# Kernel tuning notes

Measured on AMD Instinct MI355X. Metric: run time of the kernel, lower is better.

The kernel has to match this reference:

```python
import jax, jax.numpy as jnp
import numpy as np

N, D, E, OUT = 100000, 128, 600000, 128


def setup_inputs() -> dict:
    key = jax.random.key(0)
    k1, k2, k3, k4, k5 = jax.random.split(key, 5)
    x = jax.random.normal(k1, (N, D), dtype=jnp.float32)
    # Linear params (stored as [in, out]; y = h @ W + b, same math as nn.Linear)
    W = jax.random.normal(k2, (D, OUT), dtype=jnp.float32) * (1.0 / np.sqrt(D))
    b = jax.random.normal(k3, (OUT,), dtype=jnp.float32) * 0.01
    # Flattened ragged neighbor lists as COO edges: node edge_dst[e] aggregates x[edge_src[e]]
    edge_src = jax.random.randint(k4, (E,), 0, N, dtype=jnp.int32)
    edge_dst = jnp.sort(jax.random.randint(k5, (E,), 0, N, dtype=jnp.int32))
    return {"x": x, "W": W, "b": b, "edge_src": edge_src, "edge_dst": edge_dst}


def reference(x, W, b, edge_src, edge_dst):
    n = x.shape[0]
    # segment-mean of neighbor features per destination node
    neigh_sum = jax.ops.segment_sum(x[edge_src], edge_dst, num_segments=n)  # [N, D]
    deg = jax.ops.segment_sum(jnp.ones((edge_dst.shape[0],), x.dtype), edge_dst, num_segments=n)  # [N]
    # nodes with no neighbors keep zero mean (matches `if neigh:` branch)
    neigh_mean = neigh_sum / jnp.maximum(deg, 1.0)[:, None]
    h = x + neigh_mean
    return jax.nn.relu(h @ W + b)
```

## Files before the change

### kernel.cpp

```cpp
#include <hip/hip_runtime.h>
#include <hip/hip_bf16.h>


#define FD  128
#define BR  64
#define HSB 136

typedef __attribute__((ext_vector_type(8))) short bf16x8;
typedef __attribute__((ext_vector_type(4))) float f32x4;

__device__ __forceinline__ short f2bf(float f) {
    unsigned u = __float_as_uint(f);
    return (short)((u + 0x7FFFu + ((u >> 16) & 1u)) >> 16);
}
__device__ __forceinline__ float bf2f(short s) {
    return __uint_as_float(((unsigned)(unsigned short)s) << 16);
}

__global__ __launch_bounds__(256) void prep_full_kernel(
    const float* __restrict__ x, const float* __restrict__ W,
    const int* __restrict__ edst, int* __restrict__ rp,
    short* __restrict__ pkW, short* __restrict__ xb, int N, int E)
{
    const int gid = blockIdx.x * 256 + threadIdx.x;
    const int nth = gridDim.x * 256;

    const int nv = N * FD / 8;
    for (int i = gid; i < nv; i += nth) {
        float4 f0 = *(const float4*)(x + (size_t)i * 8);
        float4 f1 = *(const float4*)(x + (size_t)i * 8 + 4);
        short tmp[8] = {f2bf(f0.x), f2bf(f0.y), f2bf(f0.z), f2bf(f0.w),
                        f2bf(f1.x), f2bf(f1.y), f2bf(f1.z), f2bf(f1.w)};
        *(bf16x8*)(xb + (size_t)i * 8) = *(bf16x8*)tmp;
    }
    for (int e = gid; e < E; e += nth) {
        int cur = edst[e];
        int prev = e ? edst[e - 1] : -1;
        for (int v = prev + 1; v <= cur; ++v) rp[v] = e;
        if (e == E - 1)
            for (int v = cur + 1; v <= N; ++v) rp[v] = E;
    }
    if (gid < 2048) {
        int wave = gid >> 9, rem = gid & 511;
        int ct = rem >> 8, rem2 = rem & 255;
        int kt = rem2 >> 6, lane = rem2 & 63;
        int q = lane >> 4, lr = lane & 15;
        int col = wave * 32 + ct * 16 + lr;
        int k0 = kt * 32 + q * 8;
        short tmp[8];
#pragma unroll
        for (int e2 = 0; e2 < 8; ++e2)
            tmp[e2] = f2bf(W[(size_t)(k0 + e2) * FD + col]);
        *(bf16x8*)(pkW + (size_t)gid * 8) = *(bf16x8*)tmp;
    }
}

__global__ __launch_bounds__(256) void meanagg_main2_kernel(
    const short* __restrict__ xb, const short* __restrict__ pkW,
    const float* __restrict__ bias, const int* __restrict__ esrc,
    const int* __restrict__ rp, float* __restrict__ out, int N, int E)
{
    __shared__ short shb[BR * HSB];
    __shared__ int seg[BR + 1];

    const int t = threadIdx.x;
    const int base = blockIdx.x * BR;

    if (t < BR + 1) {
        int idx = base + t;
        seg[t] = rp[idx > N ? N : idx];
    }
    __syncthreads();

    const int wave = t >> 6;
    const int lane = t & 63;
    const int qw = lane >> 4;
    const int ql = lane & 15;
    const int qb = qw << 4;
    const int rowbase = wave * 16;

    {
        int rb0 = rowbase + qw;
        int r0  = base + rb0;
        int s = (r0 < N) ? seg[rb0] : 0;
        int e = (r0 < N) ? seg[rb0 + 1] : 0;
        int srcv_n = (s + ql < e) ? esrc[s + ql] : 0;
        bf16x8 xv_n = {0, 0, 0, 0, 0, 0, 0, 0};
        if (r0 < N) xv_n = *(const bf16x8*)(xb + (size_t)r0 * FD + 8 * ql);

        for (int it = 0; it < 4; ++it) {
            const int cur_rb = rowbase + it * 4 + qw;
            const int cur_r  = base + cur_rb;
            const int cs0 = s, ce = e;
            int srcv = srcv_n;
            const bf16x8 xv = xv_n;

            if (it < 3) {
                int nrb = rowbase + (it + 1) * 4 + qw;
                int nr  = base + nrb;
                s = (nr < N) ? seg[nrb] : 0;
                e = (nr < N) ? seg[nrb + 1] : 0;
                srcv_n = (s + ql < e) ? esrc[s + ql] : 0;
                bf16x8 z = {0, 0, 0, 0, 0, 0, 0, 0};
                xv_n = z;
                if (nr < N) xv_n = *(const bf16x8*)(xb + (size_t)nr * FD + 8 * ql);
            }

            if (cur_r < N) {
                float a[8];
#pragma unroll
                for (int p = 0; p < 8; ++p) a[p] = 0.f;

                for (int cs = cs0; cs < ce; cs += 16) {
                    int m = ce - cs; if (m > 16) m = 16;
                    if (cs != cs0)
                        srcv = (cs + ql < ce) ? esrc[cs + ql] : 0;
                    for (int j0 = 0; j0 < m; j0 += 6) {
                        uint4 v[6];
#pragma unroll
                        for (int u = 0; u < 6; ++u) {
                            int jj = j0 + u;
                            int idx = __shfl(srcv, qb + (jj & 15));
                            if (jj >= m) idx = 0;
                            v[u] = *(const uint4*)(xb + (size_t)idx * FD + 8 * ql);
                        }
#pragma unroll
                        for (int u = 0; u < 6; ++u) {
                            float f = (j0 + u < m) ? 1.f : 0.f;
                            unsigned w;
                            w = v[u].x;
                            a[0] = fmaf(__uint_as_float(w << 16), f, a[0]);
                            a[1] = fmaf(__uint_as_float(w & 0xFFFF0000u), f, a[1]);
                            w = v[u].y;
                            a[2] = fmaf(__uint_as_float(w << 16), f, a[2]);
                            a[3] = fmaf(__uint_as_float(w & 0xFFFF0000u), f, a[3]);
                            w = v[u].z;
                            a[4] = fmaf(__uint_as_float(w << 16), f, a[4]);
                            a[5] = fmaf(__uint_as_float(w & 0xFFFF0000u), f, a[5]);
                            w = v[u].w;
                            a[6] = fmaf(__uint_as_float(w << 16), f, a[6]);
                            a[7] = fmaf(__uint_as_float(w & 0xFFFF0000u), f, a[7]);
                        }
                    }
                }
                int deg = ce - cs0;
                float inv = 1.0f / (float)(deg > 0 ? deg : 1);
                short hb[8];
#pragma unroll
                for (int p = 0; p < 8; ++p)
                    hb[p] = f2bf(bf2f(xv[p]) + a[p] * inv);
                *(bf16x8*)(shb + cur_rb * HSB + 8 * ql) = *(bf16x8*)hb;
            }
        }
    }
    __syncthreads();

    const int lr = lane & 15;
    const int q  = lane >> 4;
    const int colb = wave * 32;

    bf16x8 bfr[2][4];
#pragma unroll
    for (int ct = 0; ct < 2; ++ct)
#pragma unroll
        for (int kt = 0; kt < 4; ++kt) {
            int f = ((wave * 2 + ct) * 4 + kt) * 64 + lane;
            bfr[ct][kt] = *(const bf16x8*)(pkW + (size_t)f * 8);
        }

    f32x4 acc[4][2];
#pragma unroll
    for (int rt = 0; rt < 4; ++rt) {
        acc[rt][0] = (f32x4){0.f, 0.f, 0.f, 0.f};
        acc[rt][1] = (f32x4){0.f, 0.f, 0.f, 0.f};
    }

#pragma unroll
    for (int rt = 0; rt < 4; ++rt)
#pragma unroll
        for (int kt = 0; kt < 4; ++kt) {
            bf16x8 av = *(const bf16x8*)(shb + (rt * 16 + lr) * HSB + kt * 32 + q * 8);
            acc[rt][0] = __builtin_amdgcn_mfma_f32_16x16x32_bf16(av, bfr[0][kt], acc[rt][0], 0, 0, 0);
            acc[rt][1] = __builtin_amdgcn_mfma_f32_16x16x32_bf16(av, bfr[1][kt], acc[rt][1], 0, 0, 0);
        }

    const float b0 = bias[colb + lr];
    const float b1 = bias[colb + 16 + lr];

#pragma unroll
    for (int rt = 0; rt < 4; ++rt)
#pragma unroll
        for (int j = 0; j < 4; ++j) {
            int row = base + rt * 16 + q * 4 + j;
            if (row < N) {
                float v0 = acc[rt][0][j] + b0; v0 = v0 > 0.f ? v0 : 0.f;
                float v1 = acc[rt][1][j] + b1; v1 = v1 > 0.f ? v1 : 0.f;
                out[(size_t)row * FD + colb + lr]      = v0;
                out[(size_t)row * FD + colb + 16 + lr] = v1;
            }
        }
}

__global__ __launch_bounds__(256) void prep_kernel(
    const float* __restrict__ W, const int* __restrict__ edst,
    int* __restrict__ rp, short* __restrict__ pkW, int N, int E)
{
    int gid = blockIdx.x * 256 + threadIdx.x;
    if (gid < E) {
        int cur = edst[gid];
        int prev = gid ? edst[gid - 1] : -1;
        for (int v = prev + 1; v <= cur; ++v) rp[v] = gid;
        if (gid == E - 1)
            for (int v = cur + 1; v <= N; ++v) rp[v] = E;
    }
    if (gid < 2048) {
        int wave = gid >> 9, rem = gid & 511;
        int ct = rem >> 8, rem2 = rem & 255;
        int kt = rem2 >> 6, lane = rem2 & 63;
        int q = lane >> 4, lr = lane & 15;
        int col = wave * 32 + ct * 16 + lr;
        int k0 = kt * 32 + q * 8;
        short tmp[8];
#pragma unroll
        for (int e = 0; e < 8; ++e)
            tmp[e] = f2bf(W[(size_t)(k0 + e) * FD + col]);
        *(bf16x8*)(pkW + (size_t)gid * 8) = *(bf16x8*)tmp;
    }
}

__global__ __launch_bounds__(256) void meanagg_main_kernel(
    const float* __restrict__ x, const short* __restrict__ pkW,
    const float* __restrict__ bias, const int* __restrict__ esrc,
    const int* __restrict__ rp, float* __restrict__ out, int N, int E)
{
    __shared__ short shb[BR * HSB];
    __shared__ int seg[BR + 1];

    const int t = threadIdx.x;
    const int base = blockIdx.x * BR;

    if (t < BR + 1) {
        int idx = base + t;
        seg[t] = rp[idx > N ? N : idx];
    }
    __syncthreads();

    const int wave = t >> 6;
    const int lane = t & 63;
    const int sw = lane >> 5;
    const int sl = lane & 31;
    const int lb = sw << 5;
    const int rowbase = wave * 16;

    {
        int rb0 = rowbase + sw;
        int r0  = base + rb0;
        int s0  = (r0 < N) ? seg[rb0] : 0;
        int e0  = (r0 < N) ? seg[rb0 + 1] : 0;
        int src_next = (s0 + sl < e0) ? esrc[s0 + sl] : 0;
        float4 xv_next = make_float4(0.f, 0.f, 0.f, 0.f);
        if (r0 < N) xv_next = *(const float4*)(x + (size_t)r0 * FD + 4 * sl);

        int s = s0, e = e0;
        for (int it = 0; it < 8; ++it) {
            const int cur_rb = rowbase + it * 2 + sw;
            const int cur_r  = base + cur_rb;
            const int cur_s  = s, cur_e = e;
            const int src_l  = src_next;
            const float4 xv  = xv_next;

            if (it < 7) {
                int nrb = rowbase + (it + 1) * 2 + sw;
                int nr  = base + nrb;
                s = (nr < N) ? seg[nrb] : 0;
                e = (nr < N) ? seg[nrb + 1] : 0;
                src_next = (s + sl < e) ? esrc[s + sl] : 0;
                xv_next = make_float4(0.f, 0.f, 0.f, 0.f);
                if (nr < N) xv_next = *(const float4*)(x + (size_t)nr * FD + 4 * sl);
            }

            if (cur_r < N) {
                float4 a0 = make_float4(0.f, 0.f, 0.f, 0.f), a1 = a0;
                int srcv = src_l;
                for (int cs = cur_s; cs < cur_e; cs += 32) {
                    int m = cur_e - cs; if (m > 32) m = 32;
                    if (cs != cur_s)
                        srcv = (cs + sl < cur_e) ? esrc[cs + sl] : 0;
                    for (int j0 = 0; j0 < m; j0 += 8) {
                        const int rem = m - j0;
                        float4 v[8];
#pragma unroll
                        for (int u = 0; u < 8; ++u) {
                            int idx = __shfl(srcv, lb + ((j0 + u) & 31));
                            v[u] = *(const float4*)(x + (size_t)idx * FD + 4 * sl);
                        }
#pragma unroll
                        for (int u = 0; u < 8; ++u) {
                            float f = (u < rem) ? 1.f : 0.f;
                            float4* A = (u & 1) ? &a1 : &a0;
                            A->x = fmaf(v[u].x, f, A->x);
                            A->y = fmaf(v[u].y, f, A->y);
                            A->z = fmaf(v[u].z, f, A->z);
                            A->w = fmaf(v[u].w, f, A->w);
                        }
                    }
                }
                int deg = cur_e - cur_s;
                float inv = 1.0f / (float)(deg > 0 ? deg : 1);
                short4 hb;
                hb.x = f2bf(xv.x + (a0.x + a1.x) * inv);
                hb.y = f2bf(xv.y + (a0.y + a1.y) * inv);
                hb.z = f2bf(xv.z + (a0.z + a1.z) * inv);
                hb.w = f2bf(xv.w + (a0.w + a1.w) * inv);
                *(short4*)(shb + cur_rb * HSB + 4 * sl) = hb;
            }
        }
    }
    __syncthreads();

    const int lr = lane & 15;
    const int q  = lane >> 4;
    const int colb = wave * 32;

    bf16x8 bfr[2][4];
#pragma unroll
    for (int ct = 0; ct < 2; ++ct)
#pragma unroll
        for (int kt = 0; kt < 4; ++kt) {
            int f = ((wave * 2 + ct) * 4 + kt) * 64 + lane;
            bfr[ct][kt] = *(const bf16x8*)(pkW + (size_t)f * 8);
        }

    f32x4 acc[4][2];
#pragma unroll
    for (int rt = 0; rt < 4; ++rt) {
        acc[rt][0] = (f32x4){0.f, 0.f, 0.f, 0.f};
        acc[rt][1] = (f32x4){0.f, 0.f, 0.f, 0.f};
    }

#pragma unroll
    for (int rt = 0; rt < 4; ++rt)
#pragma unroll
        for (int kt = 0; kt < 4; ++kt) {
            bf16x8 av = *(const bf16x8*)(shb + (rt * 16 + lr) * HSB + kt * 32 + q * 8);
            acc[rt][0] = __builtin_amdgcn_mfma_f32_16x16x32_bf16(av, bfr[0][kt], acc[rt][0], 0, 0, 0);
            acc[rt][1] = __builtin_amdgcn_mfma_f32_16x16x32_bf16(av, bfr[1][kt], acc[rt][1], 0, 0, 0);
        }

    const float b0 = bias[colb + lr];
    const float b1 = bias[colb + 16 + lr];

#pragma unroll
    for (int rt = 0; rt < 4; ++rt)
#pragma unroll
        for (int j = 0; j < 4; ++j) {
            int row = base + rt * 16 + q * 4 + j;
            if (row < N) {
                float v0 = acc[rt][0][j] + b0; v0 = v0 > 0.f ? v0 : 0.f;
                float v1 = acc[rt][1][j] + b1; v1 = v1 > 0.f ? v1 : 0.f;
                out[(size_t)row * FD + colb + lr]      = v0;
                out[(size_t)row * FD + colb + 16 + lr] = v1;
            }
        }
}

__global__ __launch_bounds__(256) void meanagg_fused_kernel(
    const float* __restrict__ x, const float* __restrict__ W,
    const float* __restrict__ bias, const int* __restrict__ esrc,
    const int* __restrict__ edst, float* __restrict__ out, int N, int E)
{
    __shared__ short shb[BR * HSB];
    __shared__ int seg[BR + 1];

    const int t = threadIdx.x;
    const int base = blockIdx.x * BR;

    if (t < BR + 1) {
        int v = base + t;
        int lo = 0, hi = E;
        while (lo < hi) {
            int mid = (lo + hi) >> 1;
            if (edst[mid] < v) lo = mid + 1; else hi = mid;
        }
        seg[t] = lo;
    }
    __syncthreads();

    const int wave = t >> 6;
    const int lane = t & 63;
    const int sw = lane >> 5;
    const int sl = lane & 31;
    const int lb = sw << 5;
    const int rowbase = wave * 16;

    for (int it = 0; it < 8; ++it) {
        int cur_rb = rowbase + it * 2 + sw;
        int cur_r  = base + cur_rb;
        if (cur_r >= N) break;
        int cur_s = seg[cur_rb], cur_e = seg[cur_rb + 1];
        float4 a0 = make_float4(0.f, 0.f, 0.f, 0.f), a1 = a0;
        for (int cs = cur_s; cs < cur_e; cs += 32) {
            int m = cur_e - cs; if (m > 32) m = 32;
            int srcv = (cs + sl < cur_e) ? esrc[cs + sl] : 0;
            for (int j0 = 0; j0 < m; j0 += 8) {
                const int rem = m - j0;
#pragma unroll
                for (int u = 0; u < 8; ++u) {
                    int idx = __shfl(srcv, lb + ((j0 + u) & 31));
                    float4 v = *(const float4*)(x + (size_t)idx * FD + 4 * sl);
                    float f = (u < rem) ? 1.f : 0.f;
                    float4* A = (u & 1) ? &a1 : &a0;
                    A->x = fmaf(v.x, f, A->x);
                    A->y = fmaf(v.y, f, A->y);
                    A->z = fmaf(v.z, f, A->z);
                    A->w = fmaf(v.w, f, A->w);
                }
            }
        }
        float4 xv = *(const float4*)(x + (size_t)cur_r * FD + 4 * sl);
        int deg = cur_e - cur_s;
        float inv = 1.0f / (float)(deg > 0 ? deg : 1);
        short4 hb;
        hb.x = f2bf(xv.x + (a0.x + a1.x) * inv);
        hb.y = f2bf(xv.y + (a0.y + a1.y) * inv);
        hb.z = f2bf(xv.z + (a0.z + a1.z) * inv);
        hb.w = f2bf(xv.w + (a0.w + a1.w) * inv);
        *(short4*)(shb + cur_rb * HSB + 4 * sl) = hb;
    }
    __syncthreads();

    const int lr = lane & 15;
    const int q  = lane >> 4;
    const int colb = wave * 32;

    bf16x8 bfr[2][4];
#pragma unroll
    for (int ct = 0; ct < 2; ++ct) {
        int col = colb + ct * 16 + lr;
#pragma unroll
        for (int kt = 0; kt < 4; ++kt) {
            bf16x8 f;
#pragma unroll
            for (int e = 0; e < 8; ++e)
                f[e] = f2bf(W[(size_t)(kt * 32 + q * 8 + e) * FD + col]);
            bfr[ct][kt] = f;
        }
    }

    f32x4 acc[4][2];
#pragma unroll
    for (int rt = 0; rt < 4; ++rt) {
        acc[rt][0] = (f32x4){0.f, 0.f, 0.f, 0.f};
        acc[rt][1] = (f32x4){0.f, 0.f, 0.f, 0.f};
    }

#pragma unroll
    for (int rt = 0; rt < 4; ++rt)
#pragma unroll
        for (int kt = 0; kt < 4; ++kt) {
            bf16x8 av = *(const bf16x8*)(shb + (rt * 16 + lr) * HSB + kt * 32 + q * 8);
            acc[rt][0] = __builtin_amdgcn_mfma_f32_16x16x32_bf16(av, bfr[0][kt], acc[rt][0], 0, 0, 0);
            acc[rt][1] = __builtin_amdgcn_mfma_f32_16x16x32_bf16(av, bfr[1][kt], acc[rt][1], 0, 0, 0);
        }

    const float b0 = bias[colb + lr];
    const float b1 = bias[colb + 16 + lr];

#pragma unroll
    for (int rt = 0; rt < 4; ++rt)
#pragma unroll
        for (int j = 0; j < 4; ++j) {
            int row = base + rt * 16 + q * 4 + j;
            if (row < N) {
                float v0 = acc[rt][0][j] + b0; v0 = v0 > 0.f ? v0 : 0.f;
                float v1 = acc[rt][1][j] + b1; v1 = v1 > 0.f ? v1 : 0.f;
                out[(size_t)row * FD + colb + lr]      = v0;
                out[(size_t)row * FD + colb + 16 + lr] = v1;
            }
        }
}

extern "C" void kernel_launch(void* const* d_in, const int* in_sizes, int n_in,
                              void* d_out, int out_size, void* d_ws, size_t ws_size,
                              hipStream_t stream) {
    const float* x    = (const float*)d_in[0];
    const float* W    = (const float*)d_in[1];
    const float* bias = (const float*)d_in[2];
    const int* esrc   = (const int*)d_in[3];
    const int* edst   = (const int*)d_in[4];
    float* out        = (float*)d_out;

    int N = in_sizes[0] / FD;
    int E = in_sizes[3];
    int blocks = (N + BR - 1) / BR;

    size_t rp_bytes = (size_t)(N + 1) * 4;
    size_t pk_off   = (rp_bytes + 511) & ~(size_t)511;
    size_t xb_off   = (pk_off + 2048 * 8 * 2 + 511) & ~(size_t)511;
    size_t need_med = pk_off + 2048 * 8 * 2;
    size_t need_big = xb_off + (size_t)N * FD * 2;

    if (ws_size >= need_big) {
        int* rp    = (int*)d_ws;
        short* pkW = (short*)((char*)d_ws + pk_off);
        short* xb  = (short*)((char*)d_ws + xb_off);
        prep_full_kernel<<<2048, 256, 0, stream>>>(x, W, edst, rp, pkW, xb, N, E);
        meanagg_main2_kernel<<<blocks, 256, 0, stream>>>(xb, pkW, bias, esrc, rp, out, N, E);
    } else if (ws_size >= need_med) {
        int* rp    = (int*)d_ws;
        short* pkW = (short*)((char*)d_ws + pk_off);
        int pblocks = (E + 255) / 256;
        prep_kernel<<<pblocks, 256, 0, stream>>>(W, edst, rp, pkW, N, E);
        meanagg_main_kernel<<<blocks, 256, 0, stream>>>(x, pkW, bias, esrc, rp, out, N, E);
    } else {
        meanagg_fused_kernel<<<blocks, 256, 0, stream>>>(x, W, bias, esrc, edst, out, N, E);
    }
}
```

Before: 57.65 us.

## Halve rows per block and issue both rows' neighbor gathers upfront

The main aggregation kernel now handles 32 rows per block instead of 64, which doubles the grid. Each 16-lane group processes two rows and issues the first 8 neighbor gathers for both rows before accumulating either, replacing the old sequential 4-iteration prefetch loop. Higher-degree rows fall back to a tail loop that gathers 8 at a time. The aim is more memory-level parallelism and more blocks in flight to hide gather latency. The cost is more register pressure from 16 outstanding uint4 loads, and each block loads W fragments for half as many rows.

```diff
diff --git a/kernel.cpp b/kernel.cpp
--- a/kernel.cpp
+++ b/kernel.cpp
@@ -3,7 +3,8 @@
 
 
 #define FD  128
-#define BR  64
+#define BR  32
+#define BRF 64
 #define HSB 136
 
 typedef __attribute__((ext_vector_type(8))) short bf16x8;
@@ -39,6 +40,9 @@
         for (int v = prev + 1; v <= cur; ++v) rp[v] = e;
         if (e == E - 1)
             for (int v = cur + 1; v <= N; ++v) rp[v] = E;
+    }
+    if (E == 0) {
+        for (int v = gid; v <= N; v += nth) rp[v] = 0;
     }
     if (gid < 2048) {
         int wave = gid >> 9, rem = gid & 511;
@@ -55,7 +59,76 @@
     }
 }
 
-__global__ __launch_bounds__(256) void meanagg_main2_kernel(
+__device__ __forceinline__ void issue8(const short* __restrict__ xb, int srcv,
+                                       int qb, int ql, int j0, int m, uint4 v[8])
+{
+#pragma unroll
+    for (int u = 0; u < 8; ++u) {
+        int jj = j0 + u;
+        int idx = __shfl(srcv, qb + (jj & 15));
+        if (jj >= m) idx = 0;
+        v[u] = *(const uint4*)(xb + (size_t)idx * FD + 8 * ql);
+    }
+}
+
+__device__ __forceinline__ void acc8(const uint4 v[8], int c, float2 a[4])
+{
+#pragma unroll
+    for (int u = 0; u < 8; ++u) {
+        float f = (u < c) ? 1.f : 0.f;
+        unsigned w;
+        w = v[u].x;
+        a[0].x = fmaf(__uint_as_float(w << 16), f, a[0].x);
+        a[0].y = fmaf(__uint_as_float(w & 0xFFFF0000u), f, a[0].y);
+        w = v[u].y;
+        a[1].x = fmaf(__uint_as_float(w << 16), f, a[1].x);
+        a[1].y = fmaf(__uint_as_float(w & 0xFFFF0000u), f, a[1].y);
+        w = v[u].z;
+        a[2].x = fmaf(__uint_as_float(w << 16), f, a[2].x);
+        a[2].y = fmaf(__uint_as_float(w & 0xFFFF0000u), f, a[2].y);
+        w = v[u].w;
+        a[3].x = fmaf(__uint_as_float(w << 16), f, a[3].x);
+        a[3].y = fmaf(__uint_as_float(w & 0xFFFF0000u), f, a[3].y);
+    }
+}
+
+__device__ __forceinline__ void row_tail(const short* __restrict__ xb,
+                                         const int* __restrict__ esrc,
+                                         int s, int e, int srcv,
+                                         int qb, int ql, float2 a[4])
+{
+    int deg = e - s;
+    if (deg > 8) {
+        uint4 v2[8];
+        int m16 = deg < 16 ? deg : 16;
+        issue8(xb, srcv, qb, ql, 8, m16, v2);
+        acc8(v2, m16 - 8, a);
+        for (int cs = s + 16; cs < e; cs += 16) {
+            int m = e - cs; if (m > 16) m = 16;
+            int sv = (cs + ql < e) ? esrc[cs + ql] : 0;
+            for (int j0 = 0; j0 < m; j0 += 8) {
+                issue8(xb, sv, qb, ql, j0, m, v2);
+                int c = m - j0; if (c > 8) c = 8;
+                acc8(v2, c, a);
+            }
+        }
+    }
+}
+
+__device__ __forceinline__ void finalize_row(short* shb, int rb, int ql,
+                                             const bf16x8 xv, const float2 a[4], int deg)
+{
+    float inv = 1.0f / (float)(deg > 0 ? deg : 1);
+    short hb[8];
+#pragma unroll
+    for (int k = 0; k < 4; ++k) {
+        hb[2 * k]     = f2bf(bf2f(xv[2 * k])     + a[k].x * inv);
+        hb[2 * k + 1] = f2bf(bf2f(xv[2 * k + 1]) + a[k].y * inv);
+    }
+    *(bf16x8*)(shb + rb * HSB + 8 * ql) = *(bf16x8*)hb;
+}
+
+__global__ __launch_bounds__(256) void meanagg_main3_kernel(
     const short* __restrict__ xb, const short* __restrict__ pkW,
     const float* __restrict__ bias, const int* __restrict__ esrc,
     const int* __restrict__ rp, float* __restrict__ out, int N, int E)
@@ -77,82 +150,38 @@
     const int qw = lane >> 4;
     const int ql = lane & 15;
     const int qb = qw << 4;
-    const int rowbase = wave * 16;
-
-    {
-        int rb0 = rowbase + qw;
-        int r0  = base + rb0;
-        int s = (r0 < N) ? seg[rb0] : 0;
-        int e = (r0 < N) ? seg[rb0 + 1] : 0;
-        int srcv_n = (s + ql < e) ? esrc[s + ql] : 0;
-        bf16x8 xv_n = {0, 0, 0, 0, 0, 0, 0, 0};
-        if (r0 < N) xv_n = *(const bf16x8*)(xb + (size_t)r0 * FD + 8 * ql);
-
-        for (int it = 0; it < 4; ++it) {
-            const int cur_rb = rowbase + it * 4 + qw;
-            const int cur_r  = base + cur_rb;
-            const int cs0 = s, ce = e;
-            int srcv = srcv_n;
-            const bf16x8 xv = xv_n;
-
-            if (it < 3) {
-                int nrb = rowbase + (it + 1) * 4 + qw;
-                int nr  = base + nrb;
-                s = (nr < N) ? seg[nrb] : 0;
-                e = (nr < N) ? seg[nrb + 1] : 0;
-                srcv_n = (s + ql < e) ? esrc[s + ql] : 0;
-                bf16x8 z = {0, 0, 0, 0, 0, 0, 0, 0};
-                xv_n = z;
-                if (nr < N) xv_n = *(const bf16x8*)(xb + (size_t)nr * FD + 8 * ql);
-            }
-
-            if (cur_r < N) {
-                float a[8];
-#pragma unroll
-                for (int p = 0; p < 8; ++p) a[p] = 0.f;
-
-                for (int cs = cs0; cs < ce; cs += 16) {
-                    int m = ce - cs; if (m > 16) m = 16;
-                    if (cs != cs0)
-                        srcv = (cs + ql < ce) ? esrc[cs + ql] : 0;
-                    for (int j0 = 0; j0 < m; j0 += 6) {
-                        uint4 v[6];
-#pragma unroll
-                        for (int u = 0; u < 6; ++u) {
-                            int jj = j0 + u;
-                            int idx = __shfl(srcv, qb + (jj & 15));
-                            if (jj >= m) idx = 0;
-                            v[u] = *(const uint4*)(xb + (size_t)idx * FD + 8 * ql);
-                        }
-#pragma unroll
-                        for (int u = 0; u < 6; ++u) {
-                            float f = (j0 + u < m) ? 1.f : 0.f;
-                            unsigned w;
-                            w = v[u].x;
-                            a[0] = fmaf(__uint_as_float(w << 16), f, a[0]);
-                            a[1] = fmaf(__uint_as_float(w & 0xFFFF0000u), f, a[1]);
-                            w = v[u].y;
-                            a[2] = fmaf(__uint_as_float(w << 16), f, a[2]);
-                            a[3] = fmaf(__uint_as_float(w & 0xFFFF0000u), f, a[3]);
-                            w = v[u].z;
-                            a[4] = fmaf(__uint_as_float(w << 16), f, a[4]);
-                            a[5] = fmaf(__uint_as_float(w & 0xFFFF0000u), f, a[5]);
-                            w = v[u].w;
-                            a[6] = fmaf(__uint_as_float(w << 16), f, a[6]);
-                            a[7] = fmaf(__uint_as_float(w & 0xFFFF0000u), f, a[7]);
-                        }
-                    }
-                }
-                int deg = ce - cs0;
-                float inv = 1.0f / (float)(deg > 0 ? deg : 1);
-                short hb[8];
-#pragma unroll
-                for (int p = 0; p < 8; ++p)
-                    hb[p] = f2bf(bf2f(xv[p]) + a[p] * inv);
-                *(bf16x8*)(shb + cur_rb * HSB + 8 * ql) = *(bf16x8*)hb;
-            }
-        }
-    }
+
+    const int rb0 = wave * 8 + qw;
+    const int rb1 = rb0 + 4;
+    const int r0 = base + rb0, r1 = base + rb1;
+
+    const int s0 = seg[rb0], e0 = seg[rb0 + 1];
+    const int s1 = seg[rb1], e1 = seg[rb1 + 1];
+
+    int srcv0 = (s0 + ql < e0) ? esrc[s0 + ql] : 0;
+    int srcv1 = (s1 + ql < e1) ? esrc[s1 + ql] : 0;
+    bf16x8 xv0 = {0, 0, 0, 0, 0, 0, 0, 0}, xv1 = xv0;
+    if (r0 < N) xv0 = *(const bf16x8*)(xb + (size_t)r0 * FD + 8 * ql);
+    if (r1 < N) xv1 = *(const bf16x8*)(xb + (size_t)r1 * FD + 8 * ql);
+
+    const int deg0 = e0 - s0, deg1 = e1 - s1;
+    const int m0 = deg0 < 16 ? deg0 : 16;
+    const int m1 = deg1 < 16 ? deg1 : 16;
+
+    uint4 v0[8], v1[8];
+    issue8(xb, srcv0, qb, ql, 0, m0, v0);
+    issue8(xb, srcv1, qb, ql, 0, m1, v1);
+
+    float2 a[4] = {{0.f, 0.f}, {0.f, 0.f}, {0.f, 0.f}, {0.f, 0.f}};
+    acc8(v0, m0 < 8 ? m0 : 8, a);
+    row_tail(xb, esrc, s0, e0, srcv0, qb, ql, a);
+    finalize_row(shb, rb0, ql, xv0, a, deg0);
+
+    a[0] = a[1] = a[2] = a[3] = make_float2(0.f, 0.f);
+    acc8(v1, m1 < 8 ? m1 : 8, a);
+    row_tail(xb, esrc, s1, e1, srcv1, qb, ql, a);
+    finalize_row(shb, rb1, ql, xv1, a, deg1);
+
     __syncthreads();
 
     const int lr = lane & 15;
@@ -168,15 +197,15 @@
             bfr[ct][kt] = *(const bf16x8*)(pkW + (size_t)f * 8);
         }
 
-    f32x4 acc[4][2];
-#pragma unroll
-    for (int rt = 0; rt < 4; ++rt) {
+    f32x4 acc[2][2];
+#pragma unroll
+    for (int rt = 0; rt < 2; ++rt) {
         acc[rt][0] = (f32x4){0.f, 0.f, 0.f, 0.f};
         acc[rt][1] = (f32x4){0.f, 0.f, 0.f, 0.f};
     }
 
 #pragma unroll
-    for (int rt = 0; rt < 4; ++rt)
+    for (int rt = 0; rt < 2; ++rt)
 #pragma unroll
         for (int kt = 0; kt < 4; ++kt) {
             bf16x8 av = *(const bf16x8*)(shb + (rt * 16 + lr) * HSB + kt * 32 + q * 8);
@@ -188,15 +217,15 @@
     const float b1 = bias[colb + 16 + lr];
 
 #pragma unroll
-    for (int rt = 0; rt < 4; ++rt)
+    for (int rt = 0; rt < 2; ++rt)
 #pragma unroll
         for (int j = 0; j < 4; ++j) {
             int row = base + rt * 16 + q * 4 + j;
             if (row < N) {
-                float v0 = acc[rt][0][j] + b0; v0 = v0 > 0.f ? v0 : 0.f;
-                float v1 = acc[rt][1][j] + b1; v1 = v1 > 0.f ? v1 : 0.f;
-                out[(size_t)row * FD + colb + lr]      = v0;
-                out[(size_t)row * FD + colb + 16 + lr] = v1;
+                float o0 = acc[rt][0][j] + b0; o0 = o0 > 0.f ? o0 : 0.f;
+                float o1 = acc[rt][1][j] + b1; o1 = o1 > 0.f ? o1 : 0.f;
+                out[(size_t)row * FD + colb + lr]      = o0;
+                out[(size_t)row * FD + colb + 16 + lr] = o1;
             }
         }
 }
@@ -233,156 +262,15 @@
     const float* __restrict__ bias, const int* __restrict__ esrc,
     const int* __restrict__ rp, float* __restrict__ out, int N, int E)
 {
-    __shared__ short shb[BR * HSB];
-    __shared__ int seg[BR + 1];
+    __shared__ short shb[BRF * HSB];
+    __shared__ int seg[BRF + 1];
 
     const int t = threadIdx.x;
-    const int base = blockIdx.x * BR;
-
-    if (t < BR + 1) {
+    const int base = blockIdx.x * BRF;
+
+    if (t < BRF + 1) {
         int idx = base + t;
         seg[t] = rp[idx > N ? N : idx];
-    }
-    __syncthreads();
-
-    const int wave = t >> 6;
-    const int lane = t & 63;
-    const int sw = lane >> 5;
-    const int sl = lane & 31;
-    const int lb = sw << 5;
-    const int rowbase = wave * 16;
-
-    {
-        int rb0 = rowbase + sw;
-        int r0  = base + rb0;
-        int s0  = (r0 < N) ? seg[rb0] : 0;
-        int e0  = (r0 < N) ? seg[rb0 + 1] : 0;
-        int src_next = (s0 + sl < e0) ? esrc[s0 + sl] : 0;
-        float4 xv_next = make_float4(0.f, 0.f, 0.f, 0.f);
-        if (r0 < N) xv_next = *(const float4*)(x + (size_t)r0 * FD + 4 * sl);
-
-        int s = s0, e = e0;
-        for (int it = 0; it < 8; ++it) {
-            const int cur_rb = rowbase + it * 2 + sw;
-            const int cur_r  = base + cur_rb;
-            const int cur_s  = s, cur_e = e;
-            const int src_l  = src_next;
-            const float4 xv  = xv_next;
-
-            if (it < 7) {
-                int nrb = rowbase + (it + 1) * 2 + sw;
-                int nr  = base + nrb;
-                s = (nr < N) ? seg[nrb] : 0;
-                e = (nr < N) ? seg[nrb + 1] : 0;
-                src_next = (s + sl < e) ? esrc[s + sl] : 0;
-                xv_next = make_float4(0.f, 0.f, 0.f, 0.f);
-                if (nr < N) xv_next = *(const float4*)(x + (size_t)nr * FD + 4 * sl);
-            }
-
-            if (cur_r < N) {
-                float4 a0 = make_float4(0.f, 0.f, 0.f, 0.f), a1 = a0;
-                int srcv = src_l;
-                for (int cs = cur_s; cs < cur_e; cs += 32) {
-                    int m = cur_e - cs; if (m > 32) m = 32;
-                    if (cs != cur_s)
-                        srcv = (cs + sl < cur_e) ? esrc[cs + sl] : 0;
-                    for (int j0 = 0; j0 < m; j0 += 8) {
-                        const int rem = m - j0;
-                        float4 v[8];
-#pragma unroll
-                        for (int u = 0; u < 8; ++u) {
-                            int idx = __shfl(srcv, lb + ((j0 + u) & 31));
-                            v[u] = *(const float4*)(x + (size_t)idx * FD + 4 * sl);
-                        }
-#pragma unroll
-                        for (int u = 0; u < 8; ++u) {
-                            float f = (u < rem) ? 1.f : 0.f;
-                            float4* A = (u & 1) ? &a1 : &a0;
-                            A->x = fmaf(v[u].x, f, A->x);
-                            A->y = fmaf(v[u].y, f, A->y);
-                            A->z = fmaf(v[u].z, f, A->z);
-                            A->w = fmaf(v[u].w, f, A->w);
-                        }
-                    }
-                }
-                int deg = cur_e - cur_s;
-                float inv = 1.0f / (float)(deg > 0 ? deg : 1);
-                short4 hb;
-                hb.x = f2bf(xv.x + (a0.x + a1.x) * inv);
-                hb.y = f2bf(xv.y + (a0.y + a1.y) * inv);
-                hb.z = f2bf(xv.z + (a0.z + a1.z) * inv);
-                hb.w = f2bf(xv.w + (a0.w + a1.w) * inv);
-                *(short4*)(shb + cur_rb * HSB + 4 * sl) = hb;
-            }
-        }
-    }
-    __syncthreads();
-
-    const int lr = lane & 15;
-    const int q  = lane >> 4;
-    const int colb = wave * 32;
-
-    bf16x8 bfr[2][4];
-#pragma unroll
-    for (int ct = 0; ct < 2; ++ct)
-#pragma unroll
-        for (int kt = 0; kt < 4; ++kt) {
-            int f = ((wave * 2 + ct) * 4 + kt) * 64 + lane;
-            bfr[ct][kt] = *(const bf16x8*)(pkW + (size_t)f * 8);
-        }
-
-    f32x4 acc[4][2];
-#pragma unroll
-    for (int rt = 0; rt < 4; ++rt) {
-        acc[rt][0] = (f32x4){0.f, 0.f, 0.f, 0.f};
-        acc[rt][1] = (f32x4){0.f, 0.f, 0.f, 0.f};
-    }
-
-#pragma unroll
-    for (int rt = 0; rt < 4; ++rt)
-#pragma unroll
-        for (int kt = 0; kt < 4; ++kt) {
-            bf16x8 av = *(const bf16x8*)(shb + (rt * 16 + lr) * HSB + kt * 32 + q * 8);
-            acc[rt][0] = __builtin_amdgcn_mfma_f32_16x16x32_bf16(av, bfr[0][kt], acc[rt][0], 0, 0, 0);
-            acc[rt][1] = __builtin_amdgcn_mfma_f32_16x16x32_bf16(av, bfr[1][kt], acc[rt][1], 0, 0, 0);
-        }
-
-    const float b0 = bias[colb + lr];
-    const float b1 = bias[colb + 16 + lr];
-
-#pragma unroll
-    for (int rt = 0; rt < 4; ++rt)
-#pragma unroll
-        for (int j = 0; j < 4; ++j) {
-            int row = base + rt * 16 + q * 4 + j;
-            if (row < N) {
-                float v0 = acc[rt][0][j] + b0; v0 = v0 > 0.f ? v0 : 0.f;
-                float v1 = acc[rt][1][j] + b1; v1 = v1 > 0.f ? v1 : 0.f;
-                out[(size_t)row * FD + colb + lr]      = v0;
-                out[(size_t)row * FD + colb + 16 + lr] = v1;
-            }
-        }
-}
-
-__global__ __launch_bounds__(256) void meanagg_fused_kernel(
-    const float* __restrict__ x, const float* __restrict__ W,
-    const float* __restrict__ bias, const int* __restrict__ esrc,
-    const int* __restrict__ edst, float* __restrict__ out, int N, int E)
-{
-    __shared__ short shb[BR * HSB];
-    __shared__ int seg[BR + 1];
-
-    const int t = threadIdx.x;
-    const int base = blockIdx.x * BR;
-
-    if (t < BR + 1) {
-        int v = base + t;
-        int lo = 0, hi = E;
-        while (lo < hi) {
-            int mid = (lo + hi) >> 1;
-            if (edst[mid] < v) lo = mid + 1; else hi = mid;
-        }
-        seg[t] = lo;
     }
     __syncthreads();
 
@@ -435,6 +323,117 @@
 
     bf16x8 bfr[2][4];
 #pragma unroll
+    for (int ct = 0; ct < 2; ++ct)
+#pragma unroll
+        for (int kt = 0; kt < 4; ++kt) {
+            int f = ((wave * 2 + ct) * 4 + kt) * 64 + lane;
+            bfr[ct][kt] = *(const bf16x8*)(pkW + (size_t)f * 8);
+        }
+
+    f32x4 acc[4][2];
+#pragma unroll
+    for (int rt = 0; rt < 4; ++rt) {
+        acc[rt][0] = (f32x4){0.f, 0.f, 0.f, 0.f};
+        acc[rt][1] = (f32x4){0.f, 0.f, 0.f, 0.f};
+    }
+
+#pragma unroll
+    for (int rt = 0; rt < 4; ++rt)
+#pragma unroll
+        for (int kt = 0; kt < 4; ++kt) {
+            bf16x8 av = *(const bf16x8*)(shb + (rt * 16 + lr) * HSB + kt * 32 + q * 8);
+            acc[rt][0] = __builtin_amdgcn_mfma_f32_16x16x32_bf16(av, bfr[0][kt], acc[rt][0], 0, 0, 0);
+            acc[rt][1] = __builtin_amdgcn_mfma_f32_16x16x32_bf16(av, bfr[1][kt], acc[rt][1], 0, 0, 0);
+        }
+
+    const float b0 = bias[colb + lr];
+    const float b1 = bias[colb + 16 + lr];
+
+#pragma unroll
+    for (int rt = 0; rt < 4; ++rt)
+#pragma unroll
+        for (int j = 0; j < 4; ++j) {
+            int row = base + rt * 16 + q * 4 + j;
+            if (row < N) {
+                float v0 = acc[rt][0][j] + b0; v0 = v0 > 0.f ? v0 : 0.f;
+                float v1 = acc[rt][1][j] + b1; v1 = v1 > 0.f ? v1 : 0.f;
+                out[(size_t)row * FD + colb + lr]      = v0;
+                out[(size_t)row * FD + colb + 16 + lr] = v1;
+            }
+        }
+}
+
+__global__ __launch_bounds__(256) void meanagg_fused_kernel(
+    const float* __restrict__ x, const float* __restrict__ W,
+    const float* __restrict__ bias, const int* __restrict__ esrc,
+    const int* __restrict__ edst, float* __restrict__ out, int N, int E)
+{
+    __shared__ short shb[BRF * HSB];
+    __shared__ int seg[BRF + 1];
+
+    const int t = threadIdx.x;
+    const int base = blockIdx.x * BRF;
+
+    if (t < BRF + 1) {
+        int v = base + t;
+        int lo = 0, hi = E;
+        while (lo < hi) {
+            int mid = (lo + hi) >> 1;
+            if (edst[mid] < v) lo = mid + 1; else hi = mid;
+        }
+        seg[t] = lo;
+    }
+    __syncthreads();
+
+    const int wave = t >> 6;
+    const int lane = t & 63;
+    const int sw = lane >> 5;
+    const int sl = lane & 31;
+    const int lb = sw << 5;
+    const int rowbase = wave * 16;
+
+    for (int it = 0; it < 8; ++it) {
+        int cur_rb = rowbase + it * 2 + sw;
+        int cur_r  = base + cur_rb;
+        if (cur_r >= N) break;
+        int cur_s = seg[cur_rb], cur_e = seg[cur_rb + 1];
+        float4 a0 = make_float4(0.f, 0.f, 0.f, 0.f), a1 = a0;
+        for (int cs = cur_s; cs < cur_e; cs += 32) {
+            int m = cur_e - cs; if (m > 32) m = 32;
+            int srcv = (cs + sl < cur_e) ? esrc[cs + sl] : 0;
+            for (int j0 = 0; j0 < m; j0 += 8) {
+                const int rem = m - j0;
+#pragma unroll
+                for (int u = 0; u < 8; ++u) {
+                    int idx = __shfl(srcv, lb + ((j0 + u) & 31));
+                    float4 v = *(const float4*)(x + (size_t)idx * FD + 4 * sl);
+                    float f = (u < rem) ? 1.f : 0.f;
+                    float4* A = (u & 1) ? &a1 : &a0;
+                    A->x = fmaf(v.x, f, A->x);
+                    A->y = fmaf(v.y, f, A->y);
+                    A->z = fmaf(v.z, f, A->z);
+                    A->w = fmaf(v.w, f, A->w);
+                }
+            }
+        }
+        float4 xv = *(const float4*)(x + (size_t)cur_r * FD + 4 * sl);
+        int deg = cur_e - cur_s;
+        float inv = 1.0f / (float)(deg > 0 ? deg : 1);
+        short4 hb;
+        hb.x = f2bf(xv.x + (a0.x + a1.x) * inv);
+        hb.y = f2bf(xv.y + (a0.y + a1.y) * inv);
+        hb.z = f2bf(xv.z + (a0.z + a1.z) * inv);
+        hb.w = f2bf(xv.w + (a0.w + a1.w) * inv);
+        *(short4*)(shb + cur_rb * HSB + 4 * sl) = hb;
+    }
+    __syncthreads();
+
+    const int lr = lane & 15;
+    const int q  = lane >> 4;
+    const int colb = wave * 32;
+
+    bf16x8 bfr[2][4];
+#pragma unroll
     for (int ct = 0; ct < 2; ++ct) {
         int col = colb + ct * 16 + lr;
 #pragma unroll
@@ -492,7 +491,6 @@
 
     int N = in_sizes[0] / FD;
     int E = in_sizes[3];
-    int blocks = (N + BR - 1) / BR;
 
     size_t rp_bytes = (size_t)(N + 1) * 4;
     size_t pk_off   = (rp_bytes + 511) & ~(size_t)511;
@@ -504,15 +502,18 @@
         int* rp    = (int*)d_ws;
         short* pkW = (short*)((char*)d_ws + pk_off);
         short* xb  = (short*)((char*)d_ws + xb_off);
+        int blocks = (N + BR - 1) / BR;
         prep_full_kernel<<<2048, 256, 0, stream>>>(x, W, edst, rp, pkW, xb, N, E);
-        meanagg_main2_kernel<<<blocks, 256, 0, stream>>>(xb, pkW, bias, esrc, rp, out, N, E);
+        meanagg_main3_kernel<<<blocks, 256, 0, stream>>>(xb, pkW, bias, esrc, rp, out, N, E);
     } else if (ws_size >= need_med) {
         int* rp    = (int*)d_ws;
         short* pkW = (short*)((char*)d_ws + pk_off);
+        int blocks = (N + BRF - 1) / BRF;
         int pblocks = (E + 255) / 256;
         prep_kernel<<<pblocks, 256, 0, stream>>>(W, edst, rp, pkW, N, E);
         meanagg_main_kernel<<<blocks, 256, 0, stream>>>(x, pkW, bias, esrc, rp, out, N, E);
     } else {
+        int blocks = (N + BRF - 1) / BRF;
         meanagg_fused_kernel<<<blocks, 256, 0, stream>>>(x, W, bias, esrc, edst, out, N, E);
     }
 }
```

Result: no change. 58.70 us (+1.8%).
